# Optimization experiments

Hardware: AMD Instinct MI355X
Metric: run time of the kernel (lower is better)

Reference implementation:

```python
import jax, jax.numpy as jnp
import numpy as np

B, LQ, LK, E, H = 2, 1024, 10000, 256, 8
D = E // H  # head_dim = 32


def setup_inputs() -> dict:
    key = jax.random.key(0)
    ks = jax.random.split(key, 10)
    s = 1.0 / np.sqrt(E).astype(np.float32)
    return {
        "bev_emb": jax.random.normal(ks[0], (B, LK, E), jnp.float32),
        "queries": jax.random.normal(ks[1], (B, LQ, E), jnp.float32),
        "Wq": jax.random.normal(ks[2], (E, E), jnp.float32) * s,
        "bq": jax.random.normal(ks[3], (E,), jnp.float32) * 0.01,
        "Wk": jax.random.normal(ks[4], (E, E), jnp.float32) * s,
        "bk": jax.random.normal(ks[5], (E,), jnp.float32) * 0.01,
        "Wv": jax.random.normal(ks[6], (E, E), jnp.float32) * s,
        "bv": jax.random.normal(ks[7], (E,), jnp.float32) * 0.01,
        "Wo": jax.random.normal(ks[8], (E, E), jnp.float32) * s,
        "bo": jax.random.normal(ks[9], (E,), jnp.float32) * 0.01,
    }


def reference(bev_emb, queries, Wq, bq, Wk, bk, Wv, bv, Wo, bo):
    Bn, Lq, Em = queries.shape
    Lk = bev_emb.shape[1]
    q = (queries @ Wq + bq).reshape(Bn, Lq, H, D)
    k = (bev_emb @ Wk + bk).reshape(Bn, Lk, H, D)
    v = (bev_emb @ Wv + bv).reshape(Bn, Lk, H, D)
    # NOTE: source applies no 1/sqrt(head_dim) scaling
    energy = jnp.einsum('bqhd,bkhd->bhqk', q, k)  # [B,H,Lq,Lk]
    attn = jax.nn.softmax(energy, axis=-1)
    out = jnp.einsum('bhqk,bkhd->bqhd', attn, v).reshape(Bn, Lq, Em)
    return out @ Wo + bo
```

## Files before the change

### kernel.cpp

```cpp
#include <hip/hip_runtime.h>
#include <hip/hip_bf16.h>

#define B_  2
#define LQ_ 1024
#define LK_ 10000
#define E_  256
#define H_  8
#define D_  32
#define NT_ ((LK_ + 63) / 64)
#define KVBLKS_ 625
#define QBLKS_  64

typedef __attribute__((ext_vector_type(8))) short bf16x8;
typedef __attribute__((ext_vector_type(4))) short bf16x4;
typedef __attribute__((ext_vector_type(4))) float f32x4;

#define LOG2E 1.4426950408889634f

static __device__ __forceinline__ short bfc(float x) {
  __bf16 b = (__bf16)x;
  return __builtin_bit_cast(short, b);
}
static __device__ __forceinline__ float bf2f(short s) {
  return (float)__builtin_bit_cast(__bf16, s);
}

#if __has_builtin(__builtin_amdgcn_exp2f)
static __device__ __forceinline__ float ex2(float x) {
  return __builtin_amdgcn_exp2f(x);
}
#else
static __device__ __forceinline__ float ex2(float x) { return exp2f(x); }
#endif

#if __has_builtin(__builtin_amdgcn_mfma_f32_16x16x16bf16_1k)
static __device__ __forceinline__ f32x4 mfma_pv(bf16x4 a, bf16x4 b, f32x4 c) {
  return __builtin_amdgcn_mfma_f32_16x16x16bf16_1k(a, b, c, 0, 0, 0);
}
#else
static __device__ __forceinline__ f32x4 mfma_pv(bf16x4 a, bf16x4 b, f32x4 c) {
  asm volatile("s_nop 1\n\tv_mfma_f32_16x16x16_bf16 %0, %1, %2, %0"
               : "+v"(c) : "v"(a), "v"(b));
  return c;
}
#endif

static __device__ __forceinline__ void tile_barrier() {
  __builtin_amdgcn_sched_barrier(0);
  asm volatile("s_waitcnt lgkmcnt(0)" ::: "memory");
  __builtin_amdgcn_s_barrier();
  __builtin_amdgcn_sched_barrier(0);
}

static __device__ __forceinline__ int xcd_swizzle(int flat, int nwg) {
  const int xcd = flat & 7, rest = flat >> 3;
  const int q = nwg >> 3, r = nwg & 7;
  return (xcd < r ? xcd * (q + 1) : r * (q + 1) + (xcd - r) * q) + rest;
}

static __device__ __forceinline__ void split8(const float4& a, const float4& b,
                                              bf16x8& hi, bf16x8& lo) {
  float v[8] = {a.x, a.y, a.z, a.w, b.x, b.y, b.z, b.w};
#pragma unroll
  for (int i = 0; i < 8; ++i) {
    const short h = bfc(v[i]);
    hi[i] = h;
    lo[i] = bfc(v[i] - bf2f(h));
  }
}

__global__ __launch_bounds__(256) void wtrans4(
    const float* __restrict__ W0, const float* __restrict__ W1,
    const float* __restrict__ W2, const float* __restrict__ W3,
    unsigned short* __restrict__ T0, unsigned short* __restrict__ T1,
    unsigned short* __restrict__ T2, unsigned short* __restrict__ T3) {
  const float* W;
  unsigned short* T;
  switch (blockIdx.z) {
    case 0:  W = W0; T = T0; break;
    case 1:  W = W1; T = T1; break;
    case 2:  W = W2; T = T2; break;
    default: W = W3; T = T3; break;
  }
  __shared__ float ts[16][17];
  const int tx = threadIdx.x & 15;
  const int ty = threadIdx.x >> 4;
  const int k0 = blockIdx.x * 16;
  const int n0 = blockIdx.y * 16;
  ts[ty][tx] = W[(size_t)(k0 + ty) * 256 + n0 + tx];
  __syncthreads();
  T[(size_t)(n0 + ty) * 256 + k0 + tx] = (unsigned short)bfc(ts[tx][ty]);
}

__global__ __launch_bounds__(256) void proj_all(
    const float* __restrict__ bev, const float* __restrict__ queries,
    const unsigned short* __restrict__ Wtk, const unsigned short* __restrict__ Wtv,
    const unsigned short* __restrict__ Wtq,
    const float* __restrict__ bk, const float* __restrict__ bv,
    const float* __restrict__ bq,
    unsigned short* __restrict__ kout, unsigned short* __restrict__ vout,
    float* __restrict__ qout) {
  const int lane = threadIdx.x & 63;
  const int nt   = threadIdx.x >> 6;
  const int lr   = lane & 15;
  const int oc   = lane >> 4;
  const int n0   = nt * 64;

  const bool isQ = (blockIdx.x >= KVBLKS_);
  const int  m0  = (isQ ? (int)blockIdx.x - KVBLKS_ : (int)blockIdx.x) * 32;
  const float* A = isQ ? queries : bev;
  const unsigned short* W1 = isQ ? Wtq : Wtk;

  f32x4 ac1[2][4], ac2[2][4];
#pragma unroll
  for (int s = 0; s < 2; ++s)
#pragma unroll
    for (int q = 0; q < 4; ++q) {
      ac1[s][q] = (f32x4){0.f, 0.f, 0.f, 0.f};
      ac2[s][q] = (f32x4){0.f, 0.f, 0.f, 0.f};
    }

  const float* a0p = &A[(size_t)(m0 + lr) * 256 + oc * 8];
  const float* a1p = a0p + 16 * 256;

  float4 ab[3][4];
#pragma unroll
  for (int i = 0; i < 3; ++i) {
    ab[i][0] = *(const float4*)(a0p + i * 32 + 0);
    ab[i][1] = *(const float4*)(a0p + i * 32 + 4);
    ab[i][2] = *(const float4*)(a1p + i * 32 + 0);
    ab[i][3] = *(const float4*)(a1p + i * 32 + 4);
  }

#pragma unroll
  for (int kb = 0; kb < 8; ++kb) {
    const int bk_ = kb % 3;

    const int wko = kb * 32 + oc * 8;
    bf16x8 w1[4], w2[4];
#pragma unroll
    for (int q = 0; q < 4; ++q) {
      w1[q] = *(const bf16x8*)&W1[(size_t)(n0 + q * 16 + lr) * 256 + wko];
      if (!isQ) w2[q] = *(const bf16x8*)&Wtv[(size_t)(n0 + q * 16 + lr) * 256 + wko];
    }

    bf16x8 ah0, al0, ah1, al1;
    split8(ab[bk_][0], ab[bk_][1], ah0, al0);
    split8(ab[bk_][2], ab[bk_][3], ah1, al1);

    if (kb < 5) {
      ab[bk_][0] = *(const float4*)(a0p + (kb + 3) * 32 + 0);
      ab[bk_][1] = *(const float4*)(a0p + (kb + 3) * 32 + 4);
      ab[bk_][2] = *(const float4*)(a1p + (kb + 3) * 32 + 0);
      ab[bk_][3] = *(const float4*)(a1p + (kb + 3) * 32 + 4);
    }

#pragma unroll
    for (int q = 0; q < 4; ++q) {
      ac1[0][q] = __builtin_amdgcn_mfma_f32_16x16x32_bf16(w1[q], ah0, ac1[0][q], 0, 0, 0);
      ac1[0][q] = __builtin_amdgcn_mfma_f32_16x16x32_bf16(w1[q], al0, ac1[0][q], 0, 0, 0);
      ac1[1][q] = __builtin_amdgcn_mfma_f32_16x16x32_bf16(w1[q], ah1, ac1[1][q], 0, 0, 0);
      ac1[1][q] = __builtin_amdgcn_mfma_f32_16x16x32_bf16(w1[q], al1, ac1[1][q], 0, 0, 0);
      if (!isQ) {
        ac2[0][q] = __builtin_amdgcn_mfma_f32_16x16x32_bf16(w2[q], ah0, ac2[0][q], 0, 0, 0);
        ac2[1][q] = __builtin_amdgcn_mfma_f32_16x16x32_bf16(w2[q], ah1, ac2[1][q], 0, 0, 0);
      }
    }
  }

#pragma unroll
  for (int s = 0; s < 2; ++s) {
#pragma unroll
    for (int q = 0; q < 4; ++q) {
      const int m = m0 + s * 16 + lr;
      const int n = n0 + q * 16 + oc * 4;
      if (isQ) {
        const float4 b4 = *(const float4*)&bq[n];
        float4 o;
        o.x = ac1[s][q][0] + b4.x; o.y = ac1[s][q][1] + b4.y;
        o.z = ac1[s][q][2] + b4.z; o.w = ac1[s][q][3] + b4.w;
        *(float4*)&qout[(size_t)m * 256 + n] = o;
      } else {
        const float4 bk4 = *(const float4*)&bk[n];
        const float4 bv4 = *(const float4*)&bv[n];
        ushort4 ok, ov;
        ok.x = (unsigned short)bfc(ac1[s][q][0] + bk4.x);
        ok.y = (unsigned short)bfc(ac1[s][q][1] + bk4.y);
        ok.z = (unsigned short)bfc(ac1[s][q][2] + bk4.z);
        ok.w = (unsigned short)bfc(ac1[s][q][3] + bk4.w);
        ov.x = (unsigned short)bfc(ac2[s][q][0] + bv4.x);
        ov.y = (unsigned short)bfc(ac2[s][q][1] + bv4.y);
        ov.z = (unsigned short)bfc(ac2[s][q][2] + bv4.z);
        ov.w = (unsigned short)bfc(ac2[s][q][3] + bv4.w);
        *(ushort4*)&kout[(size_t)m * 256 + n] = ok;
        *(ushort4*)&vout[(size_t)m * 256 + n] = ov;
      }
    }
  }
}

__global__ __launch_bounds__(256) void proj_o(const float* __restrict__ A,
                                              const unsigned short* __restrict__ Wt,
                                              const float* __restrict__ bias,
                                              float* __restrict__ C) {
  const int lane = threadIdx.x & 63;
  const int nt   = threadIdx.x >> 6;
  const int lr   = lane & 15;
  const int oc   = lane >> 4;
  const int n0   = nt * 64;
  const int m0   = blockIdx.x * 32;

  f32x4 acc[2][4];
#pragma unroll
  for (int s = 0; s < 2; ++s)
#pragma unroll
    for (int q = 0; q < 4; ++q) acc[s][q] = (f32x4){0.f, 0.f, 0.f, 0.f};

  const float* a0p = &A[(size_t)(m0 + lr) * 256 + oc * 8];
  const float* a1p = a0p + 16 * 256;

  float4 ab[3][4];
#pragma unroll
  for (int i = 0; i < 3; ++i) {
    ab[i][0] = *(const float4*)(a0p + i * 32 + 0);
    ab[i][1] = *(const float4*)(a0p + i * 32 + 4);
    ab[i][2] = *(const float4*)(a1p + i * 32 + 0);
    ab[i][3] = *(const float4*)(a1p + i * 32 + 4);
  }

#pragma unroll
  for (int kb = 0; kb < 8; ++kb) {
    const int bk_ = kb % 3;
    const int wko = kb * 32 + oc * 8;
    bf16x8 w[4];
#pragma unroll
    for (int q = 0; q < 4; ++q)
      w[q] = *(const bf16x8*)&Wt[(size_t)(n0 + q * 16 + lr) * 256 + wko];

    bf16x8 ah0, al0, ah1, al1;
    split8(ab[bk_][0], ab[bk_][1], ah0, al0);
    split8(ab[bk_][2], ab[bk_][3], ah1, al1);

    if (kb < 5) {
      ab[bk_][0] = *(const float4*)(a0p + (kb + 3) * 32 + 0);
      ab[bk_][1] = *(const float4*)(a0p + (kb + 3) * 32 + 4);
      ab[bk_][2] = *(const float4*)(a1p + (kb + 3) * 32 + 0);
      ab[bk_][3] = *(const float4*)(a1p + (kb + 3) * 32 + 4);
    }

#pragma unroll
    for (int q = 0; q < 4; ++q) {
      acc[0][q] = __builtin_amdgcn_mfma_f32_16x16x32_bf16(w[q], ah0, acc[0][q], 0, 0, 0);
      acc[0][q] = __builtin_amdgcn_mfma_f32_16x16x32_bf16(w[q], al0, acc[0][q], 0, 0, 0);
      acc[1][q] = __builtin_amdgcn_mfma_f32_16x16x32_bf16(w[q], ah1, acc[1][q], 0, 0, 0);
      acc[1][q] = __builtin_amdgcn_mfma_f32_16x16x32_bf16(w[q], al1, acc[1][q], 0, 0, 0);
    }
  }

#pragma unroll
  for (int s = 0; s < 2; ++s) {
#pragma unroll
    for (int q = 0; q < 4; ++q) {
      const int m = m0 + s * 16 + lr;
      const int n = n0 + q * 16 + oc * 4;
      const float4 b4 = *(const float4*)&bias[n];
      float4 o;
      o.x = acc[s][q][0] + b4.x; o.y = acc[s][q][1] + b4.y;
      o.z = acc[s][q][2] + b4.z; o.w = acc[s][q][3] + b4.w;
      *(float4*)&C[(size_t)m * 256 + n] = o;
    }
  }
}

__global__ __launch_bounds__(256, 4) void attn_mfma(const float* __restrict__ q,
                                                    const unsigned short* __restrict__ kbf,
                                                    const unsigned short* __restrict__ vbf,
                                                    float* __restrict__ Opart,
                                                    float* __restrict__ lpart,
                                                    float* __restrict__ o_direct,
                                                    int tiles_per_split, int nsplit) {
  const int nwg = 64 * gridDim.z;
  const int l   = xcd_swizzle(blockIdx.x + 8 * (blockIdx.y + 8 * blockIdx.z), nwg);
  const int qb   = l & 7;
  const int h    = (l >> 3) & 7;
  const int z    = l >> 6;
  const int s_id = z / B_;
  const int b    = z % B_;
  const int t    = threadIdx.x;
  const int lane = t & 63;
  const int w    = t >> 6;
  const int lq   = lane & 15;
  const int grp  = lane >> 4;

  __shared__ ushort Klds[2][64][64];
  __shared__ ushort Vtld[2][32][64];

  const int t0 = s_id * tiles_per_split;
  const int t1 = min(NT_, t0 + tiles_per_split);
  if (t0 >= NT_) return;

  const int qrowA = qb * 128 + w * 32 + lq;
  const int qrowB = qrowA + 16;
  bf16x8 qfA, qfB;
  {
    const float* qpA = &q[((size_t)(b * LQ_ + qrowA)) * E_ + h * D_ + grp * 8];
    const float* qpB = &q[((size_t)(b * LQ_ + qrowB)) * E_ + h * D_ + grp * 8];
    const float4 a0 = *(const float4*)qpA;
    const float4 a1 = *(const float4*)(qpA + 4);
    const float4 b0 = *(const float4*)qpB;
    const float4 b1 = *(const float4*)(qpB + 4);
    qfA[0] = bfc(a0.x * LOG2E); qfA[1] = bfc(a0.y * LOG2E);
    qfA[2] = bfc(a0.z * LOG2E); qfA[3] = bfc(a0.w * LOG2E);
    qfA[4] = bfc(a1.x * LOG2E); qfA[5] = bfc(a1.y * LOG2E);
    qfA[6] = bfc(a1.z * LOG2E); qfA[7] = bfc(a1.w * LOG2E);
    qfB[0] = bfc(b0.x * LOG2E); qfB[1] = bfc(b0.y * LOG2E);
    qfB[2] = bfc(b0.z * LOG2E); qfB[3] = bfc(b0.w * LOG2E);
    qfB[4] = bfc(b1.x * LOG2E); qfB[5] = bfc(b1.y * LOG2E);
    qfB[6] = bfc(b1.z * LOG2E); qfB[7] = bfc(b1.w * LOG2E);
  }

  const int krow_l = t >> 2;
  const int kchunk = t & 3;
  const int vkp    = t >> 3;
  const int vd     = (t & 7) * 4;

  f32x4 lAv = {0.f, 0.f, 0.f, 0.f}, lBv = {0.f, 0.f, 0.f, 0.f};
  f32x4 a0A = {0.f, 0.f, 0.f, 0.f}, a1A = {0.f, 0.f, 0.f, 0.f};
  f32x4 a0B = {0.f, 0.f, 0.f, 0.f}, a1B = {0.f, 0.f, 0.f, 0.f};

  const size_t kvrow0 = (size_t)b * LK_;

  uint4 kval; ushort4 v0, v1;
  auto load_tile = [&](int kn) {
    if (kn == NT_ - 1) {
      const int krow  = min(kn * 64 + krow_l, LK_ - 1);
      const int vrow0 = min(kn * 64 + 2 * vkp, LK_ - 1);
      const int vrow1 = min(kn * 64 + 2 * vkp + 1, LK_ - 1);
      kval = *(const uint4*)&kbf[(kvrow0 + krow) * E_ + h * D_ + kchunk * 8];
      v0 = *(const ushort4*)&vbf[(kvrow0 + vrow0) * E_ + h * D_ + vd];
      v1 = *(const ushort4*)&vbf[(kvrow0 + vrow1) * E_ + h * D_ + vd];
    } else {
      kval = *(const uint4*)&kbf[(kvrow0 + kn * 64 + krow_l) * E_ + h * D_ + kchunk * 8];
      v0 = *(const ushort4*)&vbf[(kvrow0 + kn * 64 + 2 * vkp) * E_ + h * D_ + vd];
      v1 = *(const ushort4*)&vbf[(kvrow0 + kn * 64 + 2 * vkp + 1) * E_ + h * D_ + vd];
    }
  };
  auto store_tile = [&](int buf) {
    *(uint4*)((char*)&Klds[buf][krow_l][0] + ((kchunk * 16) ^ ((krow_l & 7) << 4))) = kval;
#pragma unroll
    for (int i = 0; i < 4; ++i) {
      const int d = vd + i;
      *(ushort2*)((char*)&Vtld[buf][d][0] + ((vkp * 4) ^ ((d & 7) << 4))) =
          make_ushort2(((const unsigned short*)&v0)[i], ((const unsigned short*)&v1)[i]);
    }
  };

  load_tile(t0);
  store_tile(0);
  if (t0 + 1 < t1) load_tile(t0 + 1);
  tile_barrier();

  int cur = 0;
  for (int kt = t0; kt < t1; ++kt) {
    const int rem = LK_ - kt * 64;

    if (kt + 1 < t1) store_tile(cur ^ 1);
    if (kt + 2 < t1) load_tile(kt + 2);

    f32x4 pA[4], pB[4];
    __builtin_amdgcn_s_setprio(1);
#pragma unroll
    for (int s = 0; s < 4; ++s) {
      const int row = s * 16 + lq;
      const bf16x8 kf = *(const bf16x8*)((const char*)&Klds[cur][row][0] +
                                         ((grp * 16) ^ ((row & 7) << 4)));
      const f32x4 zero = {0.f, 0.f, 0.f, 0.f};
      pA[s] = __builtin_amdgcn_mfma_f32_16x16x32_bf16(kf, qfA, zero, 0, 0, 0);
      pB[s] = __builtin_amdgcn_mfma_f32_16x16x32_bf16(kf, qfB, zero, 0, 0, 0);
    }
    __builtin_amdgcn_s_setprio(0);

    bf16x4 pbA[4], pbB[4];
    if (rem >= 64) {
#pragma unroll
      for (int s = 0; s < 4; ++s)
#pragma unroll
        for (int r = 0; r < 4; ++r) {
          const float eA = ex2(pA[s][r]);
          const float eB = ex2(pB[s][r]);
          lAv[r] += eA; lBv[r] += eB;
          pbA[s][r] = bfc(eA); pbB[s][r] = bfc(eB);
        }
    } else {
#pragma unroll
      for (int s = 0; s < 4; ++s) {
        const bool vs = (s * 16 + grp * 4) < rem;
#pragma unroll
        for (int r = 0; r < 4; ++r) {
          const float eA = vs ? ex2(pA[s][r]) : 0.f;
          const float eB = vs ? ex2(pB[s][r]) : 0.f;
          lAv[r] += eA; lBv[r] += eB;
          pbA[s][r] = bfc(eA); pbB[s][r] = bfc(eB);
        }
      }
    }

    __builtin_amdgcn_s_setprio(1);
#pragma unroll
    for (int s = 0; s < 4; ++s) {
      {
        const int row = lq;
        const bf16x4 vf = *(const bf16x4*)((const char*)&Vtld[cur][row][0] +
                                           ((s * 32 + grp * 8) ^ ((row & 7) << 4)));
        a0A = mfma_pv(vf, pbA[s], a0A);
        a0B = mfma_pv(vf, pbB[s], a0B);
      }
      {
        const int row = 16 + lq;
        const bf16x4 vf = *(const bf16x4*)((const char*)&Vtld[cur][row][0] +
                                           ((s * 32 + grp * 8) ^ ((row & 7) << 4)));
        a1A = mfma_pv(vf, pbA[s], a1A);
        a1B = mfma_pv(vf, pbB[s], a1B);
      }
    }
    __builtin_amdgcn_s_setprio(0);

    tile_barrier();
    cur ^= 1;
  }

  float lA = (lAv[0] + lAv[1]) + (lAv[2] + lAv[3]);
  float lB = (lBv[0] + lBv[1]) + (lBv[2] + lBv[3]);
  lA += __shfl_xor(lA, 16);
  lA += __shfl_xor(lA, 32);
  lB += __shfl_xor(lB, 16);
  lB += __shfl_xor(lB, 32);

  if (nsplit == 1) {
    const float invA = 1.f / lA;
    const float invB = 1.f / lB;
    float* opA = &o_direct[((size_t)(b * LQ_ + qrowA)) * E_ + h * D_];
    float* opB = &o_direct[((size_t)(b * LQ_ + qrowB)) * E_ + h * D_];
#pragma unroll
    for (int r = 0; r < 4; ++r) {
      opA[grp * 4 + r]      = a0A[r] * invA;
      opA[16 + grp * 4 + r] = a1A[r] * invA;
      opB[grp * 4 + r]      = a0B[r] * invB;
      opB[16 + grp * 4 + r] = a1B[r] * invB;
    }
  } else {
    const size_t pbA =
        (size_t)s_id * (B_ * H_ * LQ_) + ((size_t)b * H_ + h) * LQ_ + qrowA;
    const size_t pbB = pbA + 16;
#pragma unroll
    for (int r = 0; r < 4; ++r) {
      Opart[pbA * D_ + grp * 4 + r]      = a0A[r];
      Opart[pbA * D_ + 16 + grp * 4 + r] = a1A[r];
      Opart[pbB * D_ + grp * 4 + r]      = a0B[r];
      Opart[pbB * D_ + 16 + grp * 4 + r] = a1B[r];
    }
    if (grp == 0) {
      lpart[pbA] = lA;
      lpart[pbB] = lB;
    }
  }
}

__global__ __launch_bounds__(256) void attn_merge(const float* __restrict__ Opart,
                                                  const float* __restrict__ lpart,
                                                  float* __restrict__ o, int S) {
  const int idx = blockIdx.x * 256 + threadIdx.x;
  if (idx >= B_ * LQ_ * E_) return;
  const int e   = idx & (E_ - 1);
  const int row = idx >> 8;
  const int b   = row >> 10;
  const int qq  = row & (LQ_ - 1);
  const int h   = e >> 5;
  const int d   = e & (D_ - 1);
  const size_t base   = ((size_t)b * H_ + h) * LQ_ + qq;
  const size_t stride = (size_t)B_ * H_ * LQ_;

  float lsum = 0.f, osum = 0.f;
  for (int s = 0; s < S; ++s) {
    lsum += lpart[s * stride + base];
    osum += Opart[(s * stride + base) * D_ + d];
  }
  o[idx] = osum / lsum;
}

extern "C" void kernel_launch(void* const* d_in, const int* in_sizes, int n_in,
                              void* d_out, int out_size, void* d_ws, size_t ws_size,
                              hipStream_t stream) {
  const float* bev     = (const float*)d_in[0];
  const float* queries = (const float*)d_in[1];
  const float* Wq      = (const float*)d_in[2];
  const float* bq      = (const float*)d_in[3];
  const float* Wk      = (const float*)d_in[4];
  const float* bk      = (const float*)d_in[5];
  const float* Wv      = (const float*)d_in[6];
  const float* bv      = (const float*)d_in[7];
  const float* Wo      = (const float*)d_in[8];
  const float* bo      = (const float*)d_in[9];
  float* out = (float*)d_out;

  const size_t nq = (size_t)B_ * LQ_ * E_;
  const size_t nk = (size_t)B_ * LK_ * E_;
  const size_t nw = (size_t)E_ * E_;
  float*          qws = (float*)d_ws;
  unsigned short* kbf = (unsigned short*)(qws + nq);
  unsigned short* vbf = kbf + nk;
  float*          ows = (float*)(vbf + nk);
  unsigned short* Wtq = (unsigned short*)(ows + nq);
  unsigned short* Wtk = Wtq + nw;
  unsigned short* Wtv = Wtk + nw;
  unsigned short* Wto = Wtv + nw;
  float*          opart = (float*)(Wto + nw);

  const size_t base_bytes = (nq * 2) * sizeof(float) +
                            (nk * 2 + nw * 4) * sizeof(unsigned short);
  const size_t per_split_bytes = (size_t)B_ * H_ * LQ_ * (D_ + 1) * sizeof(float);
  const int cands[5] = {12, 8, 4, 2, 1};
  int S = 1;
  for (int ci = 0; ci < 5; ++ci) {
    if (base_bytes + (size_t)cands[ci] * per_split_bytes <= ws_size) {
      S = cands[ci];
      break;
    }
  }

  wtrans4<<<dim3(16, 16, 4), 256, 0, stream>>>(Wq, Wk, Wv, Wo, Wtq, Wtk, Wtv, Wto);

  proj_all<<<dim3(KVBLKS_ + QBLKS_), 256, 0, stream>>>(
      bev, queries, Wtk, Wtv, Wtq, bk, bv, bq, kbf, vbf, qws);

  if (S <= 1) {
    attn_mfma<<<dim3(8, H_, B_), 256, 0, stream>>>(
        qws, kbf, vbf, nullptr, nullptr, ows, NT_, 1);
  } else {
    float* lpart = opart + (size_t)S * B_ * H_ * LQ_ * D_;
    const int tps = (NT_ + S - 1) / S;
    attn_mfma<<<dim3(8, H_, B_ * S), 256, 0, stream>>>(
        qws, kbf, vbf, opart, lpart, nullptr, tps, S);
    attn_merge<<<dim3((B_ * LQ_ * E_ + 255) / 256), 256, 0, stream>>>(
        opart, lpart, ows, S);
  }

  proj_o<<<dim3(QBLKS_), 256, 0, stream>>>(ows, Wto, bo, out);
}
```

Measured before the change: 114.2 us.

## Process 64 query rows per wave to reuse K/V tiles across four fragments

The attention kernel now gives each wave four 16-row query fragments instead of two, so each workgroup covers 256 query rows and the grid's x dimension is halved. Each K and V fragment read from LDS now feeds four MFMAs, which halves per-query K/V global and LDS traffic. The QK, exp and PV stages are interleaved per 16-key slice to limit live registers. To compensate, launch bounds drop to 2 blocks per SM and the maximum split count falls from 12 to 8, which lowers occupancy and parallelism in exchange for more reuse.

```diff
diff --git a/kernel.cpp b/kernel.cpp
--- a/kernel.cpp
+++ b/kernel.cpp
@@ -135,7 +135,6 @@
 #pragma unroll
   for (int kb = 0; kb < 8; ++kb) {
     const int bk_ = kb % 3;
-
     const int wko = kb * 32 + oc * 8;
     bf16x8 w1[4], w2[4];
 #pragma unroll
@@ -272,18 +271,18 @@
   }
 }
 
-__global__ __launch_bounds__(256, 4) void attn_mfma(const float* __restrict__ q,
+__global__ __launch_bounds__(256, 2) void attn_mfma(const float* __restrict__ q,
                                                     const unsigned short* __restrict__ kbf,
                                                     const unsigned short* __restrict__ vbf,
                                                     float* __restrict__ Opart,
                                                     float* __restrict__ lpart,
                                                     float* __restrict__ o_direct,
                                                     int tiles_per_split, int nsplit) {
-  const int nwg = 64 * gridDim.z;
-  const int l   = xcd_swizzle(blockIdx.x + 8 * (blockIdx.y + 8 * blockIdx.z), nwg);
-  const int qb   = l & 7;
-  const int h    = (l >> 3) & 7;
-  const int z    = l >> 6;
+  const int nwg = 32 * gridDim.z;
+  const int l   = xcd_swizzle(blockIdx.x + 4 * (blockIdx.y + 8 * blockIdx.z), nwg);
+  const int qb   = l & 3;
+  const int h    = (l >> 2) & 7;
+  const int z    = l >> 5;
   const int s_id = z / B_;
   const int b    = z % B_;
   const int t    = threadIdx.x;
@@ -299,24 +298,17 @@
   const int t1 = min(NT_, t0 + tiles_per_split);
   if (t0 >= NT_) return;
 
-  const int qrowA = qb * 128 + w * 32 + lq;
-  const int qrowB = qrowA + 16;
-  bf16x8 qfA, qfB;
-  {
-    const float* qpA = &q[((size_t)(b * LQ_ + qrowA)) * E_ + h * D_ + grp * 8];
-    const float* qpB = &q[((size_t)(b * LQ_ + qrowB)) * E_ + h * D_ + grp * 8];
-    const float4 a0 = *(const float4*)qpA;
-    const float4 a1 = *(const float4*)(qpA + 4);
-    const float4 b0 = *(const float4*)qpB;
-    const float4 b1 = *(const float4*)(qpB + 4);
-    qfA[0] = bfc(a0.x * LOG2E); qfA[1] = bfc(a0.y * LOG2E);
-    qfA[2] = bfc(a0.z * LOG2E); qfA[3] = bfc(a0.w * LOG2E);
-    qfA[4] = bfc(a1.x * LOG2E); qfA[5] = bfc(a1.y * LOG2E);
-    qfA[6] = bfc(a1.z * LOG2E); qfA[7] = bfc(a1.w * LOG2E);
-    qfB[0] = bfc(b0.x * LOG2E); qfB[1] = bfc(b0.y * LOG2E);
-    qfB[2] = bfc(b0.z * LOG2E); qfB[3] = bfc(b0.w * LOG2E);
-    qfB[4] = bfc(b1.x * LOG2E); qfB[5] = bfc(b1.y * LOG2E);
-    qfB[6] = bfc(b1.z * LOG2E); qfB[7] = bfc(b1.w * LOG2E);
+  const int qrow0 = qb * 256 + w * 64 + lq;
+  bf16x8 qf[4];
+#pragma unroll
+  for (int f = 0; f < 4; ++f) {
+    const float* qp = &q[((size_t)(b * LQ_ + qrow0 + f * 16)) * E_ + h * D_ + grp * 8];
+    const float4 x0 = *(const float4*)qp;
+    const float4 x1 = *(const float4*)(qp + 4);
+    qf[f][0] = bfc(x0.x * LOG2E); qf[f][1] = bfc(x0.y * LOG2E);
+    qf[f][2] = bfc(x0.z * LOG2E); qf[f][3] = bfc(x0.w * LOG2E);
+    qf[f][4] = bfc(x1.x * LOG2E); qf[f][5] = bfc(x1.y * LOG2E);
+    qf[f][6] = bfc(x1.z * LOG2E); qf[f][7] = bfc(x1.w * LOG2E);
   }
 
   const int krow_l = t >> 2;
@@ -324,9 +316,14 @@
   const int vkp    = t >> 3;
   const int vd     = (t & 7) * 4;
 
-  f32x4 lAv = {0.f, 0.f, 0.f, 0.f}, lBv = {0.f, 0.f, 0.f, 0.f};
-  f32x4 a0A = {0.f, 0.f, 0.f, 0.f}, a1A = {0.f, 0.f, 0.f, 0.f};
-  f32x4 a0B = {0.f, 0.f, 0.f, 0.f}, a1B = {0.f, 0.f, 0.f, 0.f};
+  f32x4 lv[4];
+  f32x4 acc0[4], acc1[4];
+#pragma unroll
+  for (int f = 0; f < 4; ++f) {
+    lv[f]   = (f32x4){0.f, 0.f, 0.f, 0.f};
+    acc0[f] = (f32x4){0.f, 0.f, 0.f, 0.f};
+    acc1[f] = (f32x4){0.f, 0.f, 0.f, 0.f};
+  }
 
   const size_t kvrow0 = (size_t)b * LK_;
 
@@ -367,101 +364,79 @@
     if (kt + 1 < t1) store_tile(cur ^ 1);
     if (kt + 2 < t1) load_tile(kt + 2);
 
-    f32x4 pA[4], pB[4];
-    __builtin_amdgcn_s_setprio(1);
 #pragma unroll
     for (int s = 0; s < 4; ++s) {
       const int row = s * 16 + lq;
       const bf16x8 kf = *(const bf16x8*)((const char*)&Klds[cur][row][0] +
                                          ((grp * 16) ^ ((row & 7) << 4)));
       const f32x4 zero = {0.f, 0.f, 0.f, 0.f};
-      pA[s] = __builtin_amdgcn_mfma_f32_16x16x32_bf16(kf, qfA, zero, 0, 0, 0);
-      pB[s] = __builtin_amdgcn_mfma_f32_16x16x32_bf16(kf, qfB, zero, 0, 0, 0);
-    }
-    __builtin_amdgcn_s_setprio(0);
-
-    bf16x4 pbA[4], pbB[4];
-    if (rem >= 64) {
-#pragma unroll
-      for (int s = 0; s < 4; ++s)
+      f32x4 p[4];
+      __builtin_amdgcn_s_setprio(1);
+#pragma unroll
+      for (int f = 0; f < 4; ++f)
+        p[f] = __builtin_amdgcn_mfma_f32_16x16x32_bf16(kf, qf[f], zero, 0, 0, 0);
+      __builtin_amdgcn_s_setprio(0);
+
+      bf16x4 pb[4];
+      const bool vs = (rem >= 64) || (s * 16 + grp * 4 < rem);
+#pragma unroll
+      for (int f = 0; f < 4; ++f) {
 #pragma unroll
         for (int r = 0; r < 4; ++r) {
-          const float eA = ex2(pA[s][r]);
-          const float eB = ex2(pB[s][r]);
-          lAv[r] += eA; lBv[r] += eB;
-          pbA[s][r] = bfc(eA); pbB[s][r] = bfc(eB);
-        }
-    } else {
-#pragma unroll
-      for (int s = 0; s < 4; ++s) {
-        const bool vs = (s * 16 + grp * 4) < rem;
-#pragma unroll
-        for (int r = 0; r < 4; ++r) {
-          const float eA = vs ? ex2(pA[s][r]) : 0.f;
-          const float eB = vs ? ex2(pB[s][r]) : 0.f;
-          lAv[r] += eA; lBv[r] += eB;
-          pbA[s][r] = bfc(eA); pbB[s][r] = bfc(eB);
+          const float e = vs ? ex2(p[f][r]) : 0.f;
+          lv[f][r] += e;
+          pb[f][r] = bfc(e);
         }
       }
-    }
-
-    __builtin_amdgcn_s_setprio(1);
-#pragma unroll
-    for (int s = 0; s < 4; ++s) {
-      {
-        const int row = lq;
-        const bf16x4 vf = *(const bf16x4*)((const char*)&Vtld[cur][row][0] +
-                                           ((s * 32 + grp * 8) ^ ((row & 7) << 4)));
-        a0A = mfma_pv(vf, pbA[s], a0A);
-        a0B = mfma_pv(vf, pbB[s], a0B);
+
+      const bf16x4 vfa = *(const bf16x4*)((const char*)&Vtld[cur][lq][0] +
+                                          ((s * 32 + grp * 8) ^ ((lq & 7) << 4)));
+      const bf16x4 vfb = *(const bf16x4*)((const char*)&Vtld[cur][16 + lq][0] +
+                                          ((s * 32 + grp * 8) ^ (((16 + lq) & 7) << 4)));
+      __builtin_amdgcn_s_setprio(1);
+#pragma unroll
+      for (int f = 0; f < 4; ++f) {
+        acc0[f] = mfma_pv(vfa, pb[f], acc0[f]);
+        acc1[f] = mfma_pv(vfb, pb[f], acc1[f]);
       }
-      {
-        const int row = 16 + lq;
-        const bf16x4 vf = *(const bf16x4*)((const char*)&Vtld[cur][row][0] +
-                                           ((s * 32 + grp * 8) ^ ((row & 7) << 4)));
-        a1A = mfma_pv(vf, pbA[s], a1A);
-        a1B = mfma_pv(vf, pbB[s], a1B);
-      }
-    }
-    __builtin_amdgcn_s_setprio(0);
+      __builtin_amdgcn_s_setprio(0);
+    }
 
     tile_barrier();
     cur ^= 1;
   }
 
-  float lA = (lAv[0] + lAv[1]) + (lAv[2] + lAv[3]);
-  float lB = (lBv[0] + lBv[1]) + (lBv[2] + lBv[3]);
-  lA += __shfl_xor(lA, 16);
-  lA += __shfl_xor(lA, 32);
-  lB += __shfl_xor(lB, 16);
-  lB += __shfl_xor(lB, 32);
+  float lsc[4];
+#pragma unroll
+  for (int f = 0; f < 4; ++f) {
+    float x = (lv[f][0] + lv[f][1]) + (lv[f][2] + lv[f][3]);
+    x += __shfl_xor(x, 16);
+    x += __shfl_xor(x, 32);
+    lsc[f] = x;
+  }
 
   if (nsplit == 1) {
-    const float invA = 1.f / lA;
-    const float invB = 1.f / lB;
-    float* opA = &o_direct[((size_t)(b * LQ_ + qrowA)) * E_ + h * D_];
-    float* opB = &o_direct[((size_t)(b * LQ_ + qrowB)) * E_ + h * D_];
-#pragma unroll
-    for (int r = 0; r < 4; ++r) {
-      opA[grp * 4 + r]      = a0A[r] * invA;
-      opA[16 + grp * 4 + r] = a1A[r] * invA;
-      opB[grp * 4 + r]      = a0B[r] * invB;
-      opB[16 + grp * 4 + r] = a1B[r] * invB;
+#pragma unroll
+    for (int f = 0; f < 4; ++f) {
+      const float inv = 1.f / lsc[f];
+      float* op = &o_direct[((size_t)(b * LQ_ + qrow0 + f * 16)) * E_ + h * D_];
+#pragma unroll
+      for (int r = 0; r < 4; ++r) {
+        op[grp * 4 + r]      = acc0[f][r] * inv;
+        op[16 + grp * 4 + r] = acc1[f][r] * inv;
+      }
     }
   } else {
-    const size_t pbA =
-        (size_t)s_id * (B_ * H_ * LQ_) + ((size_t)b * H_ + h) * LQ_ + qrowA;
-    const size_t pbB = pbA + 16;
-#pragma unroll
-    for (int r = 0; r < 4; ++r) {
-      Opart[pbA * D_ + grp * 4 + r]      = a0A[r];
-      Opart[pbA * D_ + 16 + grp * 4 + r] = a1A[r];
-      Opart[pbB * D_ + grp * 4 + r]      = a0B[r];
-      Opart[pbB * D_ + 16 + grp * 4 + r] = a1B[r];
-    }
-    if (grp == 0) {
-      lpart[pbA] = lA;
-      lpart[pbB] = lB;
+#pragma unroll
+    for (int f = 0; f < 4; ++f) {
+      const size_t pb_ = (size_t)s_id * (B_ * H_ * LQ_) +
+                         ((size_t)b * H_ + h) * LQ_ + qrow0 + f * 16;
+#pragma unroll
+      for (int r = 0; r < 4; ++r) {
+        Opart[pb_ * D_ + grp * 4 + r]      = acc0[f][r];
+        Opart[pb_ * D_ + 16 + grp * 4 + r] = acc1[f][r];
+      }
+      if (grp == 0) lpart[pb_] = lsc[f];
     }
   }
 }
@@ -519,9 +494,9 @@
   const size_t base_bytes = (nq * 2) * sizeof(float) +
                             (nk * 2 + nw * 4) * sizeof(unsigned short);
   const size_t per_split_bytes = (size_t)B_ * H_ * LQ_ * (D_ + 1) * sizeof(float);
-  const int cands[5] = {12, 8, 4, 2, 1};
+  const int cands[4] = {8, 4, 2, 1};
   int S = 1;
-  for (int ci = 0; ci < 5; ++ci) {
+  for (int ci = 0; ci < 4; ++ci) {
     if (base_bytes + (size_t)cands[ci] * per_split_bytes <= ws_size) {
       S = cands[ci];
       break;
@@ -534,12 +509,12 @@
       bev, queries, Wtk, Wtv, Wtq, bk, bv, bq, kbf, vbf, qws);
 
   if (S <= 1) {
-    attn_mfma<<<dim3(8, H_, B_), 256, 0, stream>>>(
+    attn_mfma<<<dim3(4, H_, B_), 256, 0, stream>>>(
         qws, kbf, vbf, nullptr, nullptr, ows, NT_, 1);
   } else {
     float* lpart = opart + (size_t)S * B_ * H_ * LQ_ * D_;
     const int tps = (NT_ + S - 1) / S;
-    attn_mfma<<<dim3(8, H_, B_ * S), 256, 0, stream>>>(
+    attn_mfma<<<dim3(4, H_, B_ * S), 256, 0, stream>>>(
         qws, kbf, vbf, opart, lpart, nullptr, tps, S);
     attn_merge<<<dim3((B_ * LQ_ * E_ + 255) / 256), 256, 0, stream>>>(
         opart, lpart, ows, S);
```

After: 117.0 us. 2.5% more time.

## Load K fragments directly into registers, drop K LDS staging, reduce split candidates

Applied to the files above, without the earlier changes.

The attention kernel no longer stages K tiles through shared memory. Each lane loads its MFMA K fragment straight from global memory into one of two register buffers, prefetched two tiles ahead, and the loop is unrolled by two to alternate between those buffers. This removes the K LDS writes and reads and halves LDS use, in exchange for more VGPRs and less coalesced global loads. The split-K candidate list also drops 12, so the largest split is now 8, which changes grid size and merge cost.

```diff
diff --git a/kernel.cpp b/kernel.cpp
--- a/kernel.cpp
+++ b/kernel.cpp
@@ -135,7 +135,6 @@
 #pragma unroll
   for (int kb = 0; kb < 8; ++kb) {
     const int bk_ = kb % 3;
-
     const int wko = kb * 32 + oc * 8;
     bf16x8 w1[4], w2[4];
 #pragma unroll
@@ -292,7 +291,6 @@
   const int lq   = lane & 15;
   const int grp  = lane >> 4;
 
-  __shared__ ushort Klds[2][64][64];
   __shared__ ushort Vtld[2][32][64];
 
   const int t0 = s_id * tiles_per_split;
@@ -319,10 +317,8 @@
     qfB[6] = bfc(b1.z * LOG2E); qfB[7] = bfc(b1.w * LOG2E);
   }
 
-  const int krow_l = t >> 2;
-  const int kchunk = t & 3;
-  const int vkp    = t >> 3;
-  const int vd     = (t & 7) * 4;
+  const int vkp = t >> 3;
+  const int vd  = (t & 7) * 4;
 
   f32x4 lAv = {0.f, 0.f, 0.f, 0.f}, lBv = {0.f, 0.f, 0.f, 0.f};
   f32x4 a0A = {0.f, 0.f, 0.f, 0.f}, a1A = {0.f, 0.f, 0.f, 0.f};
@@ -330,23 +326,23 @@
 
   const size_t kvrow0 = (size_t)b * LK_;
 
-  uint4 kval; ushort4 v0, v1;
-  auto load_tile = [&](int kn) {
-    if (kn == NT_ - 1) {
-      const int krow  = min(kn * 64 + krow_l, LK_ - 1);
-      const int vrow0 = min(kn * 64 + 2 * vkp, LK_ - 1);
-      const int vrow1 = min(kn * 64 + 2 * vkp + 1, LK_ - 1);
-      kval = *(const uint4*)&kbf[(kvrow0 + krow) * E_ + h * D_ + kchunk * 8];
-      v0 = *(const ushort4*)&vbf[(kvrow0 + vrow0) * E_ + h * D_ + vd];
-      v1 = *(const ushort4*)&vbf[(kvrow0 + vrow1) * E_ + h * D_ + vd];
-    } else {
-      kval = *(const uint4*)&kbf[(kvrow0 + kn * 64 + krow_l) * E_ + h * D_ + kchunk * 8];
-      v0 = *(const ushort4*)&vbf[(kvrow0 + kn * 64 + 2 * vkp) * E_ + h * D_ + vd];
-      v1 = *(const ushort4*)&vbf[(kvrow0 + kn * 64 + 2 * vkp + 1) * E_ + h * D_ + vd];
+  bf16x8 kregA[4], kregB[4];
+  auto load_k = [&](bf16x8(&kr)[4], int kn) {
+#pragma unroll
+    for (int s = 0; s < 4; ++s) {
+      const int row = min(kn * 64 + s * 16 + lq, LK_ - 1);
+      kr[s] = *(const bf16x8*)&kbf[(kvrow0 + row) * E_ + h * D_ + grp * 8];
     }
   };
-  auto store_tile = [&](int buf) {
-    *(uint4*)((char*)&Klds[buf][krow_l][0] + ((kchunk * 16) ^ ((krow_l & 7) << 4))) = kval;
+
+  ushort4 v0, v1;
+  auto load_v = [&](int kn) {
+    const int vrow0 = min(kn * 64 + 2 * vkp, LK_ - 1);
+    const int vrow1 = min(kn * 64 + 2 * vkp + 1, LK_ - 1);
+    v0 = *(const ushort4*)&vbf[(kvrow0 + vrow0) * E_ + h * D_ + vd];
+    v1 = *(const ushort4*)&vbf[(kvrow0 + vrow1) * E_ + h * D_ + vd];
+  };
+  auto store_v = [&](int buf) {
 #pragma unroll
     for (int i = 0; i < 4; ++i) {
       const int d = vd + i;
@@ -355,30 +351,23 @@
     }
   };
 
-  load_tile(t0);
-  store_tile(0);
-  if (t0 + 1 < t1) load_tile(t0 + 1);
-  tile_barrier();
-
-  int cur = 0;
-  for (int kt = t0; kt < t1; ++kt) {
+  auto body = [&](bf16x8(&kreg)[4], int kt, int cur) __attribute__((always_inline)) {
     const int rem = LK_ - kt * 64;
 
-    if (kt + 1 < t1) store_tile(cur ^ 1);
-    if (kt + 2 < t1) load_tile(kt + 2);
+    if (kt + 1 < t1) store_v(cur ^ 1);
+    if (kt + 2 < t1) load_v(kt + 2);
 
     f32x4 pA[4], pB[4];
     __builtin_amdgcn_s_setprio(1);
 #pragma unroll
     for (int s = 0; s < 4; ++s) {
-      const int row = s * 16 + lq;
-      const bf16x8 kf = *(const bf16x8*)((const char*)&Klds[cur][row][0] +
-                                         ((grp * 16) ^ ((row & 7) << 4)));
       const f32x4 zero = {0.f, 0.f, 0.f, 0.f};
-      pA[s] = __builtin_amdgcn_mfma_f32_16x16x32_bf16(kf, qfA, zero, 0, 0, 0);
-      pB[s] = __builtin_amdgcn_mfma_f32_16x16x32_bf16(kf, qfB, zero, 0, 0, 0);
+      pA[s] = __builtin_amdgcn_mfma_f32_16x16x32_bf16(kreg[s], qfA, zero, 0, 0, 0);
+      pB[s] = __builtin_amdgcn_mfma_f32_16x16x32_bf16(kreg[s], qfB, zero, 0, 0, 0);
     }
     __builtin_amdgcn_s_setprio(0);
+
+    if (kt + 2 < t1) load_k(kreg, kt + 2);
 
     bf16x4 pbA[4], pbB[4];
     if (rem >= 64) {
@@ -409,16 +398,14 @@
 #pragma unroll
     for (int s = 0; s < 4; ++s) {
       {
-        const int row = lq;
-        const bf16x4 vf = *(const bf16x4*)((const char*)&Vtld[cur][row][0] +
-                                           ((s * 32 + grp * 8) ^ ((row & 7) << 4)));
+        const bf16x4 vf = *(const bf16x4*)((const char*)&Vtld[cur][lq][0] +
+                                           ((s * 32 + grp * 8) ^ ((lq & 7) << 4)));
         a0A = mfma_pv(vf, pbA[s], a0A);
         a0B = mfma_pv(vf, pbB[s], a0B);
       }
       {
-        const int row = 16 + lq;
-        const bf16x4 vf = *(const bf16x4*)((const char*)&Vtld[cur][row][0] +
-                                           ((s * 32 + grp * 8) ^ ((row & 7) << 4)));
+        const bf16x4 vf = *(const bf16x4*)((const char*)&Vtld[cur][16 + lq][0] +
+                                           ((s * 32 + grp * 8) ^ (((16 + lq) & 7) << 4)));
         a1A = mfma_pv(vf, pbA[s], a1A);
         a1B = mfma_pv(vf, pbB[s], a1B);
       }
@@ -426,7 +413,25 @@
     __builtin_amdgcn_s_setprio(0);
 
     tile_barrier();
-    cur ^= 1;
+  };
+
+  load_k(kregA, t0);
+  load_v(t0);
+  store_v(0);
+  if (t0 + 1 < t1) {
+    load_v(t0 + 1);
+    load_k(kregB, t0 + 1);
+  }
+  tile_barrier();
+
+  int kt = t0, cur = 0;
+  while (kt < t1) {
+    body(kregA, kt, cur);
+    ++kt; cur ^= 1;
+    if (kt < t1) {
+      body(kregB, kt, cur);
+      ++kt; cur ^= 1;
+    }
   }
 
   float lA = (lAv[0] + lAv[1]) + (lAv[2] + lAv[3]);
@@ -519,9 +524,9 @@
   const size_t base_bytes = (nq * 2) * sizeof(float) +
                             (nk * 2 + nw * 4) * sizeof(unsigned short);
   const size_t per_split_bytes = (size_t)B_ * H_ * LQ_ * (D_ + 1) * sizeof(float);
-  const int cands[5] = {12, 8, 4, 2, 1};
+  const int cands[4] = {8, 4, 2, 1};
   int S = 1;
-  for (int ci = 0; ci < 5; ++ci) {
+  for (int ci = 0; ci < 4; ++ci) {
     if (base_bytes + (size_t)cands[ci] * per_split_bytes <= ws_size) {
       S = cands[ci];
       break;
```

Result: slower. 187.8 us (+64.5%).
